# Kernel optimization log

Measured on AMD Instinct MI355X. Metric: run time of the kernel, lower is better.

Reference implementation:

```python
import jax, jax.numpy as jnp
import numpy as np

QP = 127.0          # 2**(8-1)-1, signed symmetric int8
MIN_RANGE = 1e-6


def _ste_round(x):
    # round_pass: forward round, straight-through gradient
    return x + jax.lax.stop_gradient(jnp.round(x) - x)


def _quant_per_tensor(x):
    # symmetric per-tensor: scale = max|x| / Qp (grad flows through max as in source)
    scale = jnp.maximum(jnp.max(jnp.abs(x)), MIN_RANGE) / QP
    return _ste_round(x / scale), scale


def _qlinear(x2d, w, b):
    # faithful to _quantize_global (prefix_token_num=None path):
    #   out = (x_q @ w_q.T + bias) * (s_w * s_x)
    xq, sx = _quant_per_tensor(x2d)
    wq, sw = _quant_per_tensor(w)
    out = jnp.matmul(xq, wq.T) + b[None, :]
    return out * (sw * sx)


def setup_inputs() -> dict:
    key = jax.random.key(0)
    k = jax.random.split(key, 5)
    B, N, D, H = 8, 1024, 1024, 4096
    return {
        "x": jax.random.normal(k[0], (B, N, D), dtype=jnp.float32),
        "w1": jax.random.normal(k[1], (H, D), dtype=jnp.float32) * 0.02,
        "b1": jax.random.normal(k[2], (H,), dtype=jnp.float32) * 0.02,
        "w2": jax.random.normal(k[3], (D, H), dtype=jnp.float32) * 0.02,
        "b2": jax.random.normal(k[4], (D,), dtype=jnp.float32) * 0.02,
    }


def reference(x, w1, b1, w2, b2):
    B, N, D = x.shape
    h = _qlinear(x.reshape(-1, D), w1, b1)          # [B*N, H]
    h = jax.nn.gelu(h, approximate=False)            # exact GELU (nn.GELU default)
    o = _qlinear(h, w2, b2)                          # [B*N, D]
    return o.reshape(B, N, -1)
```

## Files before the change

### kernel.cpp

```cpp
#include <hip/hip_runtime.h>
#include <cstdint>
#include <cmath>

#define QP    127.0f
#define MINR  1e-6f

#define MTOK 8192
#define DDIM 1024
#define HDIM 4096

typedef __attribute__((ext_vector_type(4))) int int32x4;

__device__ __forceinline__ void gload16(const void* g, void* l) {
    __builtin_amdgcn_global_load_lds(
        (const __attribute__((address_space(1))) void*)g,
        (__attribute__((address_space(3))) void*)l, 16, 0, 0);
}

__global__ void zero_scales_kernel(float* g) {
    if (threadIdx.x < 4) g[threadIdx.x] = 0.0f;
}

__global__ void absmax_kernel(const float* __restrict__ in, int n4, float* __restrict__ gout) {
    const float4* in4 = (const float4*)in;
    int tid = blockIdx.x * blockDim.x + threadIdx.x;
    int stride = gridDim.x * blockDim.x;
    float m = 0.0f;
    for (int i = tid; i < n4; i += stride) {
        float4 v = in4[i];
        m = fmaxf(m, fmaxf(fmaxf(fabsf(v.x), fabsf(v.y)), fmaxf(fabsf(v.z), fabsf(v.w))));
    }
    #pragma unroll
    for (int off = 32; off; off >>= 1) m = fmaxf(m, __shfl_down(m, off));
    __shared__ float sm[4];
    int lane = threadIdx.x & 63, w = threadIdx.x >> 6;
    if (lane == 0) sm[w] = m;
    __syncthreads();
    if (threadIdx.x == 0) {
        float bm = fmaxf(fmaxf(sm[0], sm[1]), fmaxf(sm[2], sm[3]));
        atomicMax((int*)gout, __float_as_int(bm));
    }
}

__global__ void quant_kernel(const float* __restrict__ in, int8_t* __restrict__ out,
                             int n4, const float* __restrict__ gm) {
    const float s = fmaxf(*gm, MINR) / QP;
    const float4* in4 = (const float4*)in;
    int* out4 = (int*)out;
    int tid = blockIdx.x * blockDim.x + threadIdx.x;
    int stride = gridDim.x * blockDim.x;
    for (int i = tid; i < n4; i += stride) {
        float4 v = in4[i];
        int q0 = ((int)rintf(v.x / s)) & 255;
        int q1 = ((int)rintf(v.y / s)) & 255;
        int q2 = ((int)rintf(v.z / s)) & 255;
        int q3 = ((int)rintf(v.w / s)) & 255;
        out4[i] = q0 | (q1 << 8) | (q2 << 16) | (q3 << 24);
    }
}

template<int KD, int ND, bool GELU_EPI>
__global__ __launch_bounds__(256, 2)
void gemm_i8_kernel(const int8_t* __restrict__ A, const int8_t* __restrict__ B,
                    const float* __restrict__ bias,
                    const float* __restrict__ gmA, const float* __restrict__ gmB,
                    float* __restrict__ out, float* __restrict__ omax) {
    __shared__ int8_t lA[128 * 128];
    __shared__ int8_t lB[128 * 128];
    const int t = threadIdx.x;
    const int lane = t & 63;
    const int w = t >> 6;
    const int wm = (w >> 1) * 64;
    const int wn = (w & 1) * 64;
    const int lr = lane & 15;
    const int lg = lane >> 4;
    const int br = blockIdx.y, bc = blockIdx.x;

    const int8_t* Ab = A + (size_t)br * 128 * KD;
    const int8_t* Bb = B + (size_t)bc * 128 * KD;

    int32x4 acc[4][4] = {};

    for (int kt = 0; kt < KD / 128; ++kt) {
        #pragma unroll
        for (int i = 0; i < 4; ++i) {
            int c = t + i * 256;
            int r = c >> 3;
            int sl = c & 7;
            int sc = ((sl ^ (r & 7)) << 4);
            gload16(Ab + (size_t)r * KD + kt * 128 + sc, &lA[c * 16]);
            gload16(Bb + (size_t)r * KD + kt * 128 + sc, &lB[c * 16]);
        }
        __syncthreads();

        #pragma unroll
        for (int kk = 0; kk < 2; ++kk) {
            int32x4 af[4], bf[4];
            #pragma unroll
            for (int m = 0; m < 4; ++m) {
                int r = wm + m * 16 + lr;
                int g = kk * 4 + lg;
                af[m] = *(const int32x4*)&lA[r * 128 + ((g ^ (r & 7)) << 4)];
            }
            #pragma unroll
            for (int n = 0; n < 4; ++n) {
                int r = wn + n * 16 + lr;
                int g = kk * 4 + lg;
                bf[n] = *(const int32x4*)&lB[r * 128 + ((g ^ (r & 7)) << 4)];
            }
            #pragma unroll
            for (int m = 0; m < 4; ++m)
                #pragma unroll
                for (int n = 0; n < 4; ++n)
                    acc[m][n] = __builtin_amdgcn_mfma_i32_16x16x64_i8(af[m], bf[n], acc[m][n], 0, 0, 0);
        }
        __syncthreads();
    }

    const float sA = fmaxf(*gmA, MINR) / QP;
    const float sB = fmaxf(*gmB, MINR) / QP;
    const float s = sB * sA;
    float lmax = 0.0f;
    #pragma unroll
    for (int m = 0; m < 4; ++m) {
        #pragma unroll
        for (int n = 0; n < 4; ++n) {
            #pragma unroll
            for (int r = 0; r < 4; ++r) {
                int row = br * 128 + wm + m * 16 + lg * 4 + r;
                int col = bc * 128 + wn + n * 16 + lr;
                float f = (float)acc[m][n][r] + bias[col];
                f *= s;
                if (GELU_EPI) {
                    float gg = f * (erff(f / 1.41421356237309504880f) + 1.0f) * 0.5f;
                    out[(size_t)row * ND + col] = gg;
                    lmax = fmaxf(lmax, fabsf(gg));
                } else {
                    out[(size_t)row * ND + col] = f;
                }
            }
        }
    }
    if (GELU_EPI) {
        #pragma unroll
        for (int off = 32; off; off >>= 1) lmax = fmaxf(lmax, __shfl_down(lmax, off));
        __shared__ float red[4];
        if (lane == 0) red[w] = lmax;
        __syncthreads();
        if (t == 0) {
            float bm = fmaxf(fmaxf(red[0], red[1]), fmaxf(red[2], red[3]));
            atomicMax((int*)omax, __float_as_int(bm));
        }
    }
}

extern "C" void kernel_launch(void* const* d_in, const int* in_sizes, int n_in,
                              void* d_out, int out_size, void* d_ws, size_t ws_size,
                              hipStream_t stream) {
    const float* x  = (const float*)d_in[0];
    const float* w1 = (const float*)d_in[1];
    const float* b1 = (const float*)d_in[2];
    const float* w2 = (const float*)d_in[3];
    const float* b2 = (const float*)d_in[4];
    float* out = (float*)d_out;

    uint8_t* ws = (uint8_t*)d_ws;
    float*  gmax = (float*)ws;
    int8_t* xq   = (int8_t*)(ws + 256);
    int8_t* w1q  = xq  + (size_t)MTOK * DDIM;
    int8_t* w2q  = w1q + (size_t)HDIM * DDIM;
    int8_t* hq   = w2q + (size_t)DDIM * HDIM;
    float*  h    = (float*)(hq + (size_t)MTOK * HDIM);

    zero_scales_kernel<<<1, 64, 0, stream>>>(gmax);

    absmax_kernel<<<1024, 256, 0, stream>>>(x,  MTOK * DDIM / 4, gmax + 0);
    absmax_kernel<<<512,  256, 0, stream>>>(w1, HDIM * DDIM / 4, gmax + 1);
    absmax_kernel<<<512,  256, 0, stream>>>(w2, DDIM * HDIM / 4, gmax + 3);

    quant_kernel<<<2048, 256, 0, stream>>>(x,  xq,  MTOK * DDIM / 4, gmax + 0);
    quant_kernel<<<1024, 256, 0, stream>>>(w1, w1q, HDIM * DDIM / 4, gmax + 1);
    quant_kernel<<<1024, 256, 0, stream>>>(w2, w2q, DDIM * HDIM / 4, gmax + 3);

    gemm_i8_kernel<DDIM, HDIM, true>
        <<<dim3(HDIM / 128, MTOK / 128), 256, 0, stream>>>(xq, w1q, b1, gmax + 0, gmax + 1, h, gmax + 2);

    quant_kernel<<<4096, 256, 0, stream>>>(h, hq, MTOK * HDIM / 4, gmax + 2);

    gemm_i8_kernel<HDIM, DDIM, false>
        <<<dim3(DDIM / 128, MTOK / 128), 256, 0, stream>>>(hq, w2q, b2, gmax + 2, gmax + 3, out, nullptr);
}
```

Measured before the change: 211.0 us.

## Rewrite int8 GEMMs as 8-wave 256-row tiles with double-buffered phased pipeline

Replaces the 128x128, 4-wave int8 MFMA GEMM with a 512-thread kernel using 256xBN tiles, double-buffered LDS, and an 8-phase schedule. Each phase interleaves partial global-to-LDS loads with MFMA work, using explicit vmcnt waits, barriers and setprio. It also remaps workgroup IDs in an XCD-aware order to improve L2 locality. The goal is to hide global load latency and raise MFMA utilisation. In exchange it uses more LDS (up to 128KB) and more accumulator registers, and the hand-written waitcnt logic is fragile.

```diff
diff --git a/kernel.cpp b/kernel.cpp
--- a/kernel.cpp
+++ b/kernel.cpp
@@ -15,6 +15,18 @@
     __builtin_amdgcn_global_load_lds(
         (const __attribute__((address_space(1))) void*)g,
         (__attribute__((address_space(3))) void*)l, 16, 0, 0);
+}
+
+template<int N> __device__ __forceinline__ void wait_vmcnt() {
+    static_assert(N == 0 || N == 3 || N == 4, "add vmcnt case");
+    if constexpr (N == 0) asm volatile("s_waitcnt vmcnt(0)" ::: "memory");
+    else if constexpr (N == 3) asm volatile("s_waitcnt vmcnt(3)" ::: "memory");
+    else if constexpr (N == 4) asm volatile("s_waitcnt vmcnt(4)" ::: "memory");
+}
+
+__device__ __forceinline__ void barrier_fence() {
+    __builtin_amdgcn_s_barrier();
+    asm volatile("" ::: "memory");
 }
 
 __global__ void zero_scales_kernel(float* g) {
@@ -59,96 +71,168 @@
     }
 }
 
-template<int KD, int ND, bool GELU_EPI>
-__global__ __launch_bounds__(256, 2)
-void gemm_i8_kernel(const int8_t* __restrict__ A, const int8_t* __restrict__ B,
-                    const float* __restrict__ bias,
-                    const float* __restrict__ gmA, const float* __restrict__ gmB,
-                    float* __restrict__ out, float* __restrict__ omax) {
-    __shared__ int8_t lA[128 * 128];
-    __shared__ int8_t lB[128 * 128];
+template<int KD, int ND, int BN, bool GELU>
+__global__ __launch_bounds__(512, 2)
+void gemm8_i8(const int8_t* __restrict__ A, const int8_t* __restrict__ B,
+              const float* __restrict__ bias,
+              const float* __restrict__ gmA, const float* __restrict__ gmB,
+              float* __restrict__ out, float* __restrict__ omax) {
+    constexpr int BM = 256;
+    constexpr int KT = KD / 128;
+    constexpr int ITERS = KT / 2;
+    constexpr int LA = BM / 128;
+    constexpr int LB = BN / 128;
+    constexpr int VMC = LA + LB;
+    constexpr int QA = BM / 4;
+    constexpr int QB = BN / 8;
+    constexpr int NR = BN / 64;
+    constexpr int NQ = NR / 2;
+    constexpr int NTILES = ND / BN;
+
+    __shared__ int8_t lA[2 * BM * 128];
+    __shared__ int8_t lB[2 * BN * 128];
+    __shared__ float red[8];
+
     const int t = threadIdx.x;
     const int lane = t & 63;
     const int w = t >> 6;
-    const int wm = (w >> 1) * 64;
-    const int wn = (w & 1) * 64;
+    const int wr = w >> 2;
+    const int wc = w & 3;
     const int lr = lane & 15;
     const int lg = lane >> 4;
-    const int br = blockIdx.y, bc = blockIdx.x;
-
-    const int8_t* Ab = A + (size_t)br * 128 * KD;
-    const int8_t* Bb = B + (size_t)bc * 128 * KD;
-
-    int32x4 acc[4][4] = {};
-
-    for (int kt = 0; kt < KD / 128; ++kt) {
-        #pragma unroll
-        for (int i = 0; i < 4; ++i) {
-            int c = t + i * 256;
-            int r = c >> 3;
-            int sl = c & 7;
-            int sc = ((sl ^ (r & 7)) << 4);
-            gload16(Ab + (size_t)r * KD + kt * 128 + sc, &lA[c * 16]);
-            gload16(Bb + (size_t)r * KD + kt * 128 + sc, &lB[c * 16]);
-        }
-        __syncthreads();
-
-        #pragma unroll
-        for (int kk = 0; kk < 2; ++kk) {
-            int32x4 af[4], bf[4];
-            #pragma unroll
-            for (int m = 0; m < 4; ++m) {
-                int r = wm + m * 16 + lr;
-                int g = kk * 4 + lg;
-                af[m] = *(const int32x4*)&lA[r * 128 + ((g ^ (r & 7)) << 4)];
-            }
-            #pragma unroll
-            for (int n = 0; n < 4; ++n) {
-                int r = wn + n * 16 + lr;
-                int g = kk * 4 + lg;
-                bf[n] = *(const int32x4*)&lB[r * 128 + ((g ^ (r & 7)) << 4)];
-            }
-            #pragma unroll
-            for (int m = 0; m < 4; ++m)
-                #pragma unroll
-                for (int n = 0; n < 4; ++n)
-                    acc[m][n] = __builtin_amdgcn_mfma_i32_16x16x64_i8(af[m], bf[n], acc[m][n], 0, 0, 0);
-        }
-        __syncthreads();
-    }
+
+    const int nwg = gridDim.x;
+    const int orig = blockIdx.x;
+    const int wg = (orig & 7) * (nwg >> 3) + (orig >> 3);
+    const int bc = wg % NTILES;
+    const int br = wg / NTILES;
+
+    const int8_t* Abase = A + (size_t)br * BM * KD;
+    const int8_t* Bbase = B + (size_t)bc * BN * KD;
+
+    int offAg[2][LA], offAl[2][LA], offBg[2][LB], offBl[2][LB];
+    #pragma unroll
+    for (int h = 0; h < 2; ++h) {
+        #pragma unroll
+        for (int i = 0; i < LA; ++i) {
+            int c = i * 512 + t, r = c >> 3, sl = c & 7;
+            int gr = (r % QA) + h * QA + (r / QA) * 2 * QA;
+            offAg[h][i] = gr * KD + ((sl ^ (gr & 7)) << 4);
+            offAl[h][i] = gr * 128 + sl * 16;
+        }
+        #pragma unroll
+        for (int i = 0; i < LB; ++i) {
+            int c = i * 512 + t, r = c >> 3, sl = c & 7;
+            int gr = (r % QB) + h * QB + (r / QB) * 2 * QB;
+            offBg[h][i] = gr * KD + ((sl ^ (gr & 7)) << 4);
+            offBl[h][i] = gr * 128 + sl * 16;
+        }
+    }
+
+#define STAGE_A(kt, h, s) { _Pragma("unroll") for (int i_ = 0; i_ < LA; ++i_) \
+        gload16(Abase + (kt) * 128 + offAg[h][i_], &lA[(s) * BM * 128 + offAl[h][i_]]); }
+#define STAGE_B(kt, h, s) { _Pragma("unroll") for (int i_ = 0; i_ < LB; ++i_) \
+        gload16(Bbase + (kt) * 128 + offBg[h][i_], &lB[(s) * BN * 128 + offBl[h][i_]]); }
+
+    const int baseA0 = (wr * 128 + lr) * 128;
+    const int baseB0 = (wc * (BN / 4) + lr) * 128;
+    const int sw0 = ((0 + lg) ^ (lr & 7)) << 4;
+    const int sw1 = ((4 + lg) ^ (lr & 7)) << 4;
+
+    int32x4 acc[8][NR] = {};
+
+#define PHASE(P, ...) do {                                                           \
+        constexpr int s_ = (P) >> 2, mh_ = ((P) >> 1) & 1, nh_ = (P) & 1;            \
+        int32x4 af[4][2], bf[NQ][2];                                                 \
+        _Pragma("unroll") for (int m = 0; m < 4; ++m) {                              \
+            af[m][0] = *(const int32x4*)&lA[s_ * BM * 128 + baseA0 + (mh_ * 64 + m * 16) * 128 + sw0]; \
+            af[m][1] = *(const int32x4*)&lA[s_ * BM * 128 + baseA0 + (mh_ * 64 + m * 16) * 128 + sw1]; \
+        }                                                                            \
+        _Pragma("unroll") for (int n = 0; n < NQ; ++n) {                             \
+            bf[n][0] = *(const int32x4*)&lB[s_ * BN * 128 + baseB0 + (nh_ * QB + n * 16) * 128 + sw0]; \
+            bf[n][1] = *(const int32x4*)&lB[s_ * BN * 128 + baseB0 + (nh_ * QB + n * 16) * 128 + sw1]; \
+        }                                                                            \
+        __VA_ARGS__;                                                                 \
+        barrier_fence();                                                             \
+        asm volatile("s_waitcnt lgkmcnt(0)" ::: "memory");                           \
+        __builtin_amdgcn_s_setprio(1);                                               \
+        _Pragma("unroll") for (int m = 0; m < 4; ++m)                                \
+            _Pragma("unroll") for (int n = 0; n < NQ; ++n) {                         \
+                acc[mh_ * 4 + m][nh_ * NQ + n] = __builtin_amdgcn_mfma_i32_16x16x64_i8( \
+                    af[m][0], bf[n][0], acc[mh_ * 4 + m][nh_ * NQ + n], 0, 0, 0);    \
+                acc[mh_ * 4 + m][nh_ * NQ + n] = __builtin_amdgcn_mfma_i32_16x16x64_i8( \
+                    af[m][1], bf[n][1], acc[mh_ * 4 + m][nh_ * NQ + n], 0, 0, 0);    \
+            }                                                                        \
+        __builtin_amdgcn_s_setprio(0);                                               \
+    } while (0)
+
+    STAGE_A(0, 0, 0); STAGE_B(0, 0, 0); STAGE_A(0, 1, 0); STAGE_B(0, 1, 0);
+    STAGE_A(1, 0, 1); STAGE_B(1, 0, 1);
+    wait_vmcnt<VMC>();
+    barrier_fence();
+
+    for (int it = 0; it < ITERS; ++it) {
+        const int k0 = 2 * it;
+        const bool more = (it < ITERS - 1);
+
+        PHASE(0, STAGE_A(k0 + 1, 1, 1));
+        barrier_fence();
+        PHASE(1, STAGE_B(k0 + 1, 1, 1));
+        barrier_fence();
+        PHASE(2, if (more) STAGE_A(k0 + 2, 0, 0));
+        barrier_fence();
+        PHASE(3, if (more) STAGE_B(k0 + 2, 0, 0));
+        if (more) wait_vmcnt<VMC>(); else wait_vmcnt<0>();
+        barrier_fence();
+        PHASE(4, if (more) STAGE_A(k0 + 2, 1, 0));
+        barrier_fence();
+        PHASE(5, if (more) STAGE_B(k0 + 2, 1, 0));
+        barrier_fence();
+        PHASE(6, if (more) STAGE_A(k0 + 3, 0, 1));
+        barrier_fence();
+        PHASE(7, if (more) STAGE_B(k0 + 3, 0, 1));
+        wait_vmcnt<VMC>();
+        barrier_fence();
+    }
+#undef PHASE
+#undef STAGE_A
+#undef STAGE_B
 
     const float sA = fmaxf(*gmA, MINR) / QP;
     const float sB = fmaxf(*gmB, MINR) / QP;
-    const float s = sB * sA;
+    const float sc = sB * sA;
     float lmax = 0.0f;
+    const int rowb = br * BM + wr * 128 + lg * 4;
+    const int colb = bc * BN + wc * (BN / 4) + lr;
     #pragma unroll
-    for (int m = 0; m < 4; ++m) {
-        #pragma unroll
-        for (int n = 0; n < 4; ++n) {
+    for (int m = 0; m < 8; ++m) {
+        #pragma unroll
+        for (int n = 0; n < NR; ++n) {
             #pragma unroll
             for (int r = 0; r < 4; ++r) {
-                int row = br * 128 + wm + m * 16 + lg * 4 + r;
-                int col = bc * 128 + wn + n * 16 + lr;
+                int row = rowb + m * 16 + r;
+                int col = colb + n * 16;
                 float f = (float)acc[m][n][r] + bias[col];
-                f *= s;
-                if (GELU_EPI) {
-                    float gg = f * (erff(f / 1.41421356237309504880f) + 1.0f) * 0.5f;
-                    out[(size_t)row * ND + col] = gg;
-                    lmax = fmaxf(lmax, fabsf(gg));
+                f *= sc;
+                if (GELU) {
+                    float g = f * (erff(f / 1.41421356237309504880f) + 1.0f) * 0.5f;
+                    out[(size_t)row * ND + col] = g;
+                    lmax = fmaxf(lmax, fabsf(g));
                 } else {
                     out[(size_t)row * ND + col] = f;
                 }
             }
         }
     }
-    if (GELU_EPI) {
+    if (GELU) {
         #pragma unroll
         for (int off = 32; off; off >>= 1) lmax = fmaxf(lmax, __shfl_down(lmax, off));
-        __shared__ float red[4];
         if (lane == 0) red[w] = lmax;
         __syncthreads();
         if (t == 0) {
-            float bm = fmaxf(fmaxf(red[0], red[1]), fmaxf(red[2], red[3]));
+            float bm = red[0];
+            #pragma unroll
+            for (int i = 1; i < 8; ++i) bm = fmaxf(bm, red[i]);
             atomicMax((int*)omax, __float_as_int(bm));
         }
     }
@@ -182,11 +266,11 @@
     quant_kernel<<<1024, 256, 0, stream>>>(w1, w1q, HDIM * DDIM / 4, gmax + 1);
     quant_kernel<<<1024, 256, 0, stream>>>(w2, w2q, DDIM * HDIM / 4, gmax + 3);
 
-    gemm_i8_kernel<DDIM, HDIM, true>
-        <<<dim3(HDIM / 128, MTOK / 128), 256, 0, stream>>>(xq, w1q, b1, gmax + 0, gmax + 1, h, gmax + 2);
+    gemm8_i8<DDIM, HDIM, 256, true>
+        <<<512, 512, 0, stream>>>(xq, w1q, b1, gmax + 0, gmax + 1, h, gmax + 2);
 
     quant_kernel<<<4096, 256, 0, stream>>>(h, hq, MTOK * HDIM / 4, gmax + 2);
 
-    gemm_i8_kernel<HDIM, DDIM, false>
-        <<<dim3(DDIM / 128, MTOK / 128), 256, 0, stream>>>(hq, w2q, b2, gmax + 2, gmax + 3, out, nullptr);
-}
+    gemm8_i8<HDIM, DDIM, 128, false>
+        <<<256, 512, 0, stream>>>(hq, w2q, b2, gmax + 2, gmax + 3, out, nullptr);
+}
```

Result: slower. 238.5 us (+13.1%).
